# Kernel optimization log

Hardware: AMD Instinct MI355X
Metric: run time of the kernel (lower is better)

Reference implementation:

```python
import jax, jax.numpy as jnp
import numpy as np

K_PERIODS = 6


def setup_inputs() -> dict:
    key = jax.random.key(0)
    x = jax.random.normal(key, (16, 2048, 128), dtype=jnp.float32)
    return {"x": x}


def reference(x):
    # x: [B, T, N] -> out: [B, K, Pmax, N].
    # Pmax is data-dependent in the torch original (max selected period); here we
    # use the static upper bound Pmax = T so shapes are jit-static. Columns
    # p >= P_row are zero, matching the original's zero padding.
    B, T, N = x.shape
    BN = B * N
    seqs = jnp.transpose(x, (0, 2, 1)).reshape(BN, T)  # [BN, T]

    # --- top-k nonzero frequencies by spectral energy ---
    spec = jnp.fft.rfft(seqs, axis=-1)
    mag2 = spec.real ** 2 + spec.imag ** 2
    mag2 = mag2.at[:, 0].set(0.0)  # kill DC bin
    k = min(K_PERIODS, mag2.shape[-1] - 1)
    _, kidx = jax.lax.top_k(mag2, k)          # [BN, K]
    kidx = jnp.maximum(kidx, 1)

    # --- per-(row, freq) period geometry ---
    P = jnp.maximum(T // kidx, 1)             # [BN, K] period length
    cycles = jnp.maximum(T // P, 1)           # [BN, K] number of full cycles
    take = cycles * P
    base = jnp.maximum(T - take, 0)           # [BN, K] start offset

    # --- fold-and-average via scatter-add (no [BN,K,Cmax,Pmax] blowup) ---
    # element at time t >= base maps to phase p = (t - base) % P, averaged over cycles
    t = jnp.arange(T, dtype=jnp.int32)
    rel = t[None, None, :] - base[:, :, None]          # [BN, K, T]
    valid = rel >= 0
    p = jnp.where(valid, rel % P[:, :, None], 0)       # phase index in [0, P)
    vals = jnp.where(valid, seqs[:, None, :], 0.0)     # [BN, K, T]

    row = jnp.arange(BN * k, dtype=jnp.int32).reshape(BN, k, 1)
    seg_ids = row * T + p                               # flat segment id
    sums = jax.ops.segment_sum(vals.reshape(-1), seg_ids.reshape(-1),
                               num_segments=BN * k * T)
    seg = sums.reshape(BN, k, T) / cycles[:, :, None].astype(vals.dtype)

    out = seg.reshape(B, N, k, T).transpose(0, 2, 3, 1)  # [B, K, Pmax=T, N]
    return out
```

## Files before the change

kernel.cpp:

```cpp
#include <hip/hip_runtime.h>
#include <stdint.h>

#define TB   256
#define TLEN 2048
#define NB   16
#define NCH  128
#define BN   (NB*NCH)
#define KP   6

typedef unsigned long long u64;

__device__ inline float2 cmul(float2 a, float2 b) {
  return make_float2(a.x * b.x - a.y * b.y, a.x * b.y + a.y * b.x);
}
__device__ inline float2 cadd(float2 a, float2 b) { return make_float2(a.x + b.x, a.y + b.y); }
__device__ inline float2 csub(float2 a, float2 b) { return make_float2(a.x - b.x, a.y - b.y); }
__device__ inline float2 cmni(float2 a) { return make_float2(a.y, -a.x); }

#define PAD(o) ((o) + ((o) >> 4))
#define C2 0.70710678118654752f

__device__ inline void radix8(const float2 A[8], float2 w1, float2 B[8]) {
  float2 s02 = cadd(A[0], A[4]), d02 = csub(A[0], A[4]);
  float2 s13 = cadd(A[2], A[6]), d13 = csub(A[2], A[6]);
  float2 E0 = cadd(s02, s13), E1 = cadd(d02, cmni(d13));
  float2 E2 = csub(s02, s13), E3 = csub(d02, cmni(d13));
  float2 t02 = cadd(A[1], A[5]), e02 = csub(A[1], A[5]);
  float2 t13 = cadd(A[3], A[7]), e13 = csub(A[3], A[7]);
  float2 O0 = cadd(t02, t13), O1 = cadd(e02, cmni(e13));
  float2 O2 = csub(t02, t13), O3 = csub(e02, cmni(e13));
  float2 T0 = O0;
  float2 T1 = make_float2(C2 * (O1.x + O1.y), C2 * (O1.y - O1.x));
  float2 T2 = cmni(O2);
  float2 T3 = make_float2(C2 * (O3.y - O3.x), -C2 * (O3.x + O3.y));
  float2 b0 = cadd(E0, T0), b4 = csub(E0, T0);
  float2 b1 = cadd(E1, T1), b5 = csub(E1, T1);
  float2 b2 = cadd(E2, T2), b6 = csub(E2, T2);
  float2 b3 = cadd(E3, T3), b7 = csub(E3, T3);
  float2 w2 = cmul(w1, w1);
  float2 w3 = cmul(w2, w1);
  float2 w4 = cmul(w2, w2);
  float2 w5 = cmul(w4, w1);
  float2 w6 = cmul(w4, w2);
  float2 w7 = cmul(w4, w3);
  B[0] = b0;
  B[1] = cmul(w1, b1);
  B[2] = cmul(w2, b2);
  B[3] = cmul(w3, b3);
  B[4] = cmul(w4, b4);
  B[5] = cmul(w5, b5);
  B[6] = cmul(w6, b6);
  B[7] = cmul(w7, b7);
}

__global__ __launch_bounds__(256) void k_transpose(const float* __restrict__ x,
                                                   float* __restrict__ seqs) {
  __shared__ float tile[64][65];
  int bid = blockIdx.x;
  int tb = bid & 31, nb = (bid >> 5) & 1, b = bid >> 6;
  int t0 = tb * 64, n0 = nb * 64;
  int tx = threadIdx.x & 63, ty = threadIdx.x >> 6;
#pragma unroll
  for (int tt = ty; tt < 64; tt += 4)
    tile[tt][tx] = x[(size_t)(b * TLEN + t0 + tt) * NCH + n0 + tx];
  __syncthreads();
#pragma unroll
  for (int nn = ty; nn < 64; nn += 4)
    seqs[(size_t)(b * NCH + n0 + nn) * TLEN + t0 + tx] = tile[tx][nn];
}

__global__ __launch_bounds__(256, 4) void k_fft_fold(const float* __restrict__ seqs,
                                                     float* __restrict__ seg,
                                                     int* __restrict__ Pg) {
  __shared__ __align__(16) float2 bufA[2176];
  __shared__ __align__(16) float2 bufB[2176];
  __shared__ float2 tw[256];
  __shared__ u64 wmax[4];
  __shared__ int4 prm[2][KP];
  int tid = threadIdx.x, lane = tid & 63, wv = tid >> 6;
  int r0 = blockIdx.x * 2;
  const float* row0 = seqs + (size_t)r0 * TLEN;

#pragma unroll
  for (int kk = 0; kk < 8; kk++) {
    int t = tid + kk * TB;
    bufA[PAD(t)] = make_float2(row0[t], row0[t + TLEN]);
  }
  {
    float sn, cs;
    sincosf((-6.283185307179586f / 2048.f) * (float)tid, &sn, &cs);
    tw[tid & 255] = make_float2(cs, sn);
  }

#pragma unroll
  for (int stage = 0; stage < 3; stage++) {
    int s = (stage == 0) ? 1 : (stage == 1) ? 8 : 64;
    float2* xb = (stage == 1) ? bufB : bufA;
    float2* yb = (stage == 1) ? bufA : bufB;
    __syncthreads();
    int i = tid;
    int q = i & (s - 1);
    int cb = i - q;
    float2 A[8], B[8];
#pragma unroll
    for (int j = 0; j < 8; j++) A[j] = xb[PAD(i + j * 256)];
    radix8(A, tw[cb], B);
    int o = q + 8 * cb;
#pragma unroll
    for (int j = 0; j < 8; j++) yb[PAD(o + j * s)] = B[j];
  }
  __syncthreads();
#pragma unroll
  for (int ii = 0; ii < 2; ii++) {
    int i = tid + ii * TB;
    float2 a0 = bufB[PAD(i)], a1 = bufB[PAD(i + 512)];
    float2 a2 = bufB[PAD(i + 1024)], a3 = bufB[PAD(i + 1536)];
    float2 S02 = cadd(a0, a2), D02 = csub(a0, a2);
    float2 S13 = cadd(a1, a3), D13 = csub(a1, a3);
    bufA[PAD(i)]        = cadd(S02, S13);
    bufA[PAD(i + 512)]  = cadd(D02, cmni(D13));
    bufA[PAD(i + 1024)] = csub(S02, S13);
    bufA[PAD(i + 1536)] = csub(D02, cmni(D13));
  }
  __syncthreads();

  u64 kra[4], krb[4];
#pragma unroll
  for (int ii = 0; ii < 4; ii++) {
    int i = tid + ii * TB;
    int kb = i + 1;
    float2 zk = bufA[PAD(kb)];
    float2 zc = bufA[PAD(2048 - kb)];
    float ax = zk.x + zc.x, ay = zk.y - zc.y;
    float bx = zk.x - zc.x, by = zk.y + zc.y;
    float m2a = ax * ax + ay * ay;
    float m2b = bx * bx + by * by;
    kra[ii] = ((u64)__float_as_uint(m2a) << 32) | (unsigned)(0xFFFFFFFFu - (unsigned)kb);
    krb[ii] = ((u64)__float_as_uint(m2b) << 32) | (unsigned)(0xFFFFFFFFu - (unsigned)kb);
  }
  __syncthreads();
  u64* keys = (u64*)bufA;
#pragma unroll
  for (int ii = 0; ii < 4; ii++) {
    int i = tid + ii * TB;
    keys[i] = kra[ii];
    keys[1024 + i] = krb[ii];
  }
  {
    const float4* s4 = (const float4*)row0;
    float4* r4 = (float4*)bufB;
#pragma unroll
    for (int ii = 0; ii < 4; ii++) r4[tid + ii * TB] = s4[tid + ii * TB];
  }
  __syncthreads();

  int rw2 = wv >> 1;
  u64* kb2 = keys + rw2 * 1024;
  int t2 = tid & 127;
  for (int r = 0; r < KP; r++) {
    u64 best = 0ull;
    for (int i = t2; i < 1024; i += 128) {
      u64 v = kb2[i];
      best = v > best ? v : best;
    }
    for (int off = 32; off > 0; off >>= 1) {
      u64 o = __shfl_down(best, off);
      best = o > best ? o : best;
    }
    if (lane == 0) wmax[wv] = best;
    __syncthreads();
    if (t2 == 0) {
      u64 b0 = wmax[rw2 * 2], b1 = wmax[rw2 * 2 + 1];
      best = b0 > b1 ? b0 : b1;
      int bin = (int)(0xFFFFFFFFu - (unsigned)(best & 0xFFFFFFFFull));
      if (bin < 1 || bin > 1024) bin = 1;
      kb2[bin - 1] = 0ull;
      int P = TLEN / bin;
      int cyc = TLEN / P;
      int base = TLEN - cyc * P;
      prm[rw2][r] = make_int4(P, base, cyc, 0);
      Pg[(r0 + rw2) * KP + r] = P;
    }
    __syncthreads();
  }

  float* srows = (float*)bufB;
  for (int task = wv; task < 2 * KP; task += 4) {
    int rw = task & 1, k = task >> 1;
    int4 pr = prm[rw][k];
    int P = pr.x, base = pr.y, cyc = pr.z;
    float inv = 1.0f / (float)cyc;
    const float* srow = srows + rw * TLEN;
    float* dst = seg + ((size_t)(r0 + rw) * KP + k) * TLEN;

    if (P >= 64) {
      for (int p = lane; p < P; p += 64) {
        const float* sp = srow + base + p;
        float s = 0.f;
        for (int c = 0; c < cyc; c++) s += sp[c * P];
        dst[p] = s * inv;
      }
    } else {
      int wc = 64 / P, u = wc * P, ci = lane / P;
      float v = 0.f;
      if (lane < u) {
        for (int c0 = 0; c0 < cyc; c0 += wc) {
          int c = c0 + ci;
          if (c < cyc) v += srow[base + c0 * P + lane];
        }
      }
      for (int s = P; s < u; s <<= 1) {
        float o = __shfl_down(v, s);
        if (lane + s < u) v += o;
      }
      if (lane < P) dst[lane] = v * inv;
    }
  }
}

__global__ __launch_bounds__(256) void k_expand(const float* __restrict__ seg,
                                                const int* __restrict__ Pg,
                                                float4* __restrict__ out4) {
  __shared__ int Parr[NCH];
  __shared__ int Pmax_s;
  int z = blockIdx.x;
  int pc = z & 15, bk = z >> 4;
  int b = bk / KP, k = bk - KP * b;
  int tid = threadIdx.x;
  if (tid < NCH) Parr[tid] = Pg[(b * NCH + tid) * KP + k];
  __syncthreads();
  if (tid < 64) {
    int m = max(Parr[tid], Parr[tid + 64]);
    for (int off = 32; off > 0; off >>= 1) {
      int o = __shfl_down(m, off);
      m = o > m ? o : m;
    }
    if (tid == 0) Pmax_s = m;
  }
  __syncthreads();
  int p0 = pc * 128;
  int Pmax = Pmax_s;
  float4 z4 = make_float4(0.f, 0.f, 0.f, 0.f);
  size_t obase = (size_t)bk * TLEN * (NCH / 4);
  if (p0 >= Pmax) {
    for (int e = tid; e < 4096; e += TB)
      out4[obase + (size_t)(p0 + (e >> 5)) * (NCH / 4) + (e & 31)] = z4;
  } else {
    for (int e = tid; e < 4096; e += TB) {
      int p = p0 + (e >> 5);
      float4 v = z4;
      if (p < Pmax) {
        int n4 = (e & 31) * 4;
        float* vp = &v.x;
#pragma unroll
        for (int c = 0; c < 4; c++) {
          int n = n4 + c;
          if (p < Parr[n])
            vp[c] = seg[((size_t)(b * NCH + n) * KP + k) * TLEN + p];
        }
      }
      out4[obase + (size_t)p * (NCH / 4) + (e & 31)] = v;
    }
  }
}

extern "C" void kernel_launch(void* const* d_in, const int* in_sizes, int n_in,
                              void* d_out, int out_size, void* d_ws, size_t ws_size,
                              hipStream_t stream) {
  const float* x = (const float*)d_in[0];
  float* out = (float*)d_out;
  char* ws = (char*)d_ws;

  const size_t seqs_bytes = (size_t)BN * TLEN * 4;
  const size_t seg_bytes  = (size_t)BN * KP * TLEN * 4;
  float* seqs = (float*)ws;
  float* seg  = (float*)(ws + seqs_bytes);
  int* Pg     = (int*)(ws + seqs_bytes + seg_bytes);

  k_transpose<<<1024, 256, 0, stream>>>(x, seqs);
  k_fft_fold<<<BN / 2, 256, 0, stream>>>(seqs, seg, Pg);
  k_expand<<<NB * KP * 16, 256, 0, stream>>>(seg, Pg, (float4*)out);
}
```

Baseline: 157.8 us.

## Fuse transpose and expand into FFT-fold kernel, writing output directly after memset

Removes the separate transpose and expand kernels. The FFT kernel now reads two adjacent channels straight from x as float2 with a strided gather, and writes folded period averages directly into the final [B,K,T,N] layout. A memset zeroes the padding beforehand. This drops the seqs and seg intermediate round-trips through global memory and two launches. In exchange, the fold writes become scattered across the stride-N output, and the memset writes the full output once more.

Result: faster. 146.9 us (-6.9%).

```diff
diff --git a/kernel.cpp b/kernel.cpp
--- a/kernel.cpp
+++ b/kernel.cpp
@@ -53,25 +53,8 @@
   B[7] = cmul(w7, b7);
 }
 
-__global__ __launch_bounds__(256) void k_transpose(const float* __restrict__ x,
-                                                   float* __restrict__ seqs) {
-  __shared__ float tile[64][65];
-  int bid = blockIdx.x;
-  int tb = bid & 31, nb = (bid >> 5) & 1, b = bid >> 6;
-  int t0 = tb * 64, n0 = nb * 64;
-  int tx = threadIdx.x & 63, ty = threadIdx.x >> 6;
-#pragma unroll
-  for (int tt = ty; tt < 64; tt += 4)
-    tile[tt][tx] = x[(size_t)(b * TLEN + t0 + tt) * NCH + n0 + tx];
-  __syncthreads();
-#pragma unroll
-  for (int nn = ty; nn < 64; nn += 4)
-    seqs[(size_t)(b * NCH + n0 + nn) * TLEN + t0 + tx] = tile[tx][nn];
-}
-
-__global__ __launch_bounds__(256, 4) void k_fft_fold(const float* __restrict__ seqs,
-                                                     float* __restrict__ seg,
-                                                     int* __restrict__ Pg) {
+__global__ __launch_bounds__(256, 4) void k_fft_fold(const float* __restrict__ x,
+                                                     float* __restrict__ out) {
   __shared__ __align__(16) float2 bufA[2176];
   __shared__ __align__(16) float2 bufB[2176];
   __shared__ float2 tw[256];
@@ -79,12 +62,16 @@
   __shared__ int4 prm[2][KP];
   int tid = threadIdx.x, lane = tid & 63, wv = tid >> 6;
   int r0 = blockIdx.x * 2;
-  const float* row0 = seqs + (size_t)r0 * TLEN;
-
+  int b = r0 >> 7, n0 = r0 & 127;
+
+  const float2* x2 = (const float2*)x;
+  size_t xbase = (size_t)b * TLEN * 64 + (n0 >> 1);
+  float2 raw[8];
 #pragma unroll
   for (int kk = 0; kk < 8; kk++) {
     int t = tid + kk * TB;
-    bufA[PAD(t)] = make_float2(row0[t], row0[t + TLEN]);
+    raw[kk] = x2[xbase + (size_t)t * 64];
+    bufA[PAD(t)] = raw[kk];
   }
   {
     float sn, cs;
@@ -138,6 +125,13 @@
     kra[ii] = ((u64)__float_as_uint(m2a) << 32) | (unsigned)(0xFFFFFFFFu - (unsigned)kb);
     krb[ii] = ((u64)__float_as_uint(m2b) << 32) | (unsigned)(0xFFFFFFFFu - (unsigned)kb);
   }
+  float* srows = (float*)bufB;
+#pragma unroll
+  for (int kk = 0; kk < 8; kk++) {
+    int t = tid + kk * TB;
+    srows[t] = raw[kk].x;
+    srows[TLEN + t] = raw[kk].y;
+  }
   __syncthreads();
   u64* keys = (u64*)bufA;
 #pragma unroll
@@ -145,12 +139,6 @@
     int i = tid + ii * TB;
     keys[i] = kra[ii];
     keys[1024 + i] = krb[ii];
-  }
-  {
-    const float4* s4 = (const float4*)row0;
-    float4* r4 = (float4*)bufB;
-#pragma unroll
-    for (int ii = 0; ii < 4; ii++) r4[tid + ii * TB] = s4[tid + ii * TB];
   }
   __syncthreads();
 
@@ -179,26 +167,25 @@
       int cyc = TLEN / P;
       int base = TLEN - cyc * P;
       prm[rw2][r] = make_int4(P, base, cyc, 0);
-      Pg[(r0 + rw2) * KP + r] = P;
     }
     __syncthreads();
   }
 
-  float* srows = (float*)bufB;
   for (int task = wv; task < 2 * KP; task += 4) {
     int rw = task & 1, k = task >> 1;
     int4 pr = prm[rw][k];
     int P = pr.x, base = pr.y, cyc = pr.z;
     float inv = 1.0f / (float)cyc;
     const float* srow = srows + rw * TLEN;
-    float* dst = seg + ((size_t)(r0 + rw) * KP + k) * TLEN;
+    int n = n0 + rw;
+    float* dst = out + (size_t)(b * KP + k) * TLEN * NCH + n;
 
     if (P >= 64) {
       for (int p = lane; p < P; p += 64) {
         const float* sp = srow + base + p;
         float s = 0.f;
         for (int c = 0; c < cyc; c++) s += sp[c * P];
-        dst[p] = s * inv;
+        dst[(size_t)p * NCH] = s * inv;
       }
     } else {
       int wc = 64 / P, u = wc * P, ci = lane / P;
@@ -213,53 +200,7 @@
         float o = __shfl_down(v, s);
         if (lane + s < u) v += o;
       }
-      if (lane < P) dst[lane] = v * inv;
-    }
-  }
-}
-
-__global__ __launch_bounds__(256) void k_expand(const float* __restrict__ seg,
-                                                const int* __restrict__ Pg,
-                                                float4* __restrict__ out4) {
-  __shared__ int Parr[NCH];
-  __shared__ int Pmax_s;
-  int z = blockIdx.x;
-  int pc = z & 15, bk = z >> 4;
-  int b = bk / KP, k = bk - KP * b;
-  int tid = threadIdx.x;
-  if (tid < NCH) Parr[tid] = Pg[(b * NCH + tid) * KP + k];
-  __syncthreads();
-  if (tid < 64) {
-    int m = max(Parr[tid], Parr[tid + 64]);
-    for (int off = 32; off > 0; off >>= 1) {
-      int o = __shfl_down(m, off);
-      m = o > m ? o : m;
-    }
-    if (tid == 0) Pmax_s = m;
-  }
-  __syncthreads();
-  int p0 = pc * 128;
-  int Pmax = Pmax_s;
-  float4 z4 = make_float4(0.f, 0.f, 0.f, 0.f);
-  size_t obase = (size_t)bk * TLEN * (NCH / 4);
-  if (p0 >= Pmax) {
-    for (int e = tid; e < 4096; e += TB)
-      out4[obase + (size_t)(p0 + (e >> 5)) * (NCH / 4) + (e & 31)] = z4;
-  } else {
-    for (int e = tid; e < 4096; e += TB) {
-      int p = p0 + (e >> 5);
-      float4 v = z4;
-      if (p < Pmax) {
-        int n4 = (e & 31) * 4;
-        float* vp = &v.x;
-#pragma unroll
-        for (int c = 0; c < 4; c++) {
-          int n = n4 + c;
-          if (p < Parr[n])
-            vp[c] = seg[((size_t)(b * NCH + n) * KP + k) * TLEN + p];
-        }
-      }
-      out4[obase + (size_t)p * (NCH / 4) + (e & 31)] = v;
+      if (lane < P) dst[(size_t)lane * NCH] = v * inv;
     }
   }
 }
@@ -269,15 +210,8 @@
                               hipStream_t stream) {
   const float* x = (const float*)d_in[0];
   float* out = (float*)d_out;
-  char* ws = (char*)d_ws;
-
-  const size_t seqs_bytes = (size_t)BN * TLEN * 4;
-  const size_t seg_bytes  = (size_t)BN * KP * TLEN * 4;
-  float* seqs = (float*)ws;
-  float* seg  = (float*)(ws + seqs_bytes);
-  int* Pg     = (int*)(ws + seqs_bytes + seg_bytes);
-
-  k_transpose<<<1024, 256, 0, stream>>>(x, seqs);
-  k_fft_fold<<<BN / 2, 256, 0, stream>>>(seqs, seg, Pg);
-  k_expand<<<NB * KP * 16, 256, 0, stream>>>(seg, Pg, (float4*)out);
-}
+  (void)d_ws; (void)ws_size;
+
+  hipMemsetAsync(out, 0, (size_t)out_size * sizeof(float), stream);
+  k_fft_fold<<<BN / 2, 256, 0, stream>>>(x, out);
+}
```
